# Optimization experiments

Measured on AMD Instinct MI355X. Metric: run time of the kernel, lower is better.

The kernel has to match this reference:

```python
import jax, jax.numpy as jnp
import numpy as np
import math

B, CF, H, W = 2, 64, 256, 256
CH = 32          # 'channel' init arg
KS, DIL, PAD = 3, 2, 2
IMG_H, IMG_W = 512, 512


def _pos_encode(h, w, d_model):
    # Sinusoidal encoding along x and y, interleaved sin/cos -> [2*d_model, h, w]
    div = jnp.exp(jnp.arange(0, d_model, 2, dtype=jnp.float32) * (-math.log(10000.0) / d_model))  # [d/2]
    ax = jnp.arange(w, dtype=jnp.float32)[None, :] * div[:, None]   # [d/2, w]
    ay = jnp.arange(h, dtype=jnp.float32)[None, :] * div[:, None]   # [d/2, h]
    x = jnp.stack([jnp.sin(ax), jnp.cos(ax)], axis=1).reshape(d_model, w)  # even=sin, odd=cos
    y = jnp.stack([jnp.sin(ay), jnp.cos(ay)], axis=1).reshape(d_model, h)
    x = jnp.broadcast_to(x[:, None, :], (d_model, h, w))
    y = jnp.broadcast_to(y[:, :, None], (d_model, h, w))
    return jnp.concatenate([x, y], axis=0)  # [2*d_model, h, w]


def _unfold3x3(x):
    # F.unfold(kernel=3, dilation=2, padding=2, stride=1) -> [B, C, 9, H, W]
    b, c, h, w = x.shape
    xp = jnp.pad(x, ((0, 0), (0, 0), (PAD, PAD), (PAD, PAD)))
    offs = (0, DIL, 2 * DIL)
    patches = [xp[:, :, i:i + h, j:j + w] for i in offs for j in offs]  # row-major kernel order
    return jnp.stack(patches, axis=2)


def setup_inputs() -> dict:
    key = jax.random.key(0)
    k1, k2, k3, k4, k5 = jax.random.split(key, 5)
    return {
        "inp": jax.random.normal(k1, (B, CF, H, W), dtype=jnp.float32),
        "img": jax.random.uniform(k2, (B, 3, IMG_H, IMG_W), dtype=jnp.float32),
        "w_pos": jax.random.normal(k3, (CH, 2 * CH), dtype=jnp.float32) * 0.1,
        "w_img": jax.random.normal(k4, (CH, 3), dtype=jnp.float32) * 0.1,
        "w_comp": jax.random.normal(k5, (CF,), dtype=jnp.float32) * 0.1,
    }


def reference(inp, img, w_pos, w_img, w_comp):
    b, cf, h, w = inp.shape
    # positional embedding -> 1x1 conv (channel matmul)
    pos = _pos_encode(h, w, CH)                                   # [2*CH, H, W]
    pos_embd = jnp.einsum('oc,chw->ohw', w_pos, pos)              # [CH, H, W]
    pos_embd = jnp.broadcast_to(pos_embd[None], (b, CH, h, w))
    # bilinear resize of image to feature resolution, then 1x1 conv
    rimg = jax.image.resize(img, (b, 3, h, w), method='bilinear')
    rimg = jnp.einsum('oc,bchw->bohw', w_img, rimg)               # [B, CH, H, W]
    em = jnp.concatenate([rimg, pos_embd], axis=1)                # [B, 2*CH, H, W]
    # neighborhood similarity score
    un_em = _unfold3x3(em)                                        # [B, 2CH, 9, H, W]
    feature_score = jnp.einsum('bckhw,bchw->bkhw', un_em, em)     # [B, 9, H, W]
    # feature compatibility: 1x1 conv (dot with w_comp) per neighbor, sigmoid
    un_fea = _unfold3x3(inp)                                      # [B, CF, 9, H, W]
    comp_score = jax.nn.sigmoid(jnp.einsum('bckhw,c->bkhw', un_fea, w_comp))
    phi = comp_score * feature_score                              # [B, 9, H, W]
    weighted_fea = jnp.einsum('bckhw,bkhw->bchw', un_fea, phi)    # [B, CF, H, W]
    return weighted_fea
```

## Files before the change

### kernel.cpp

```cpp
#include <hip/hip_runtime.h>
#include <math.h>

namespace {
constexpr int Bn = 2, CF = 64;
constexpr int H = 256, W = 256, HW = H * W;
constexpr int IH = 512, IW = 512;

constexpr int OFF_MT   = 0;
constexpr int OFF_GXX  = OFF_MT + 256 * 256;
constexpr int OFF_GYY  = OFF_GXX + 3 * 256;
constexpr int OFF_G    = OFF_GYY + 3 * 256;
constexpr int OFF_RIMG = OFF_G + 16;
constexpr int OFF_S    = OFF_RIMG + Bn * 3 * HW;
constexpr int OFF_PX   = OFF_RIMG;
constexpr int OFF_PY   = OFF_RIMG + 32 * 256;
}

__global__ __launch_bounds__(256) void pxy_kernel(
    const float* __restrict__ w_pos,
    float* __restrict__ PX, float* __restrict__ PY)
{
  const int t = threadIdx.x;
  const int o = blockIdx.x;
  float s[16], c[16];
#pragma unroll
  for (int i = 0; i < 16; i++) {
    float d = expf((float)(2 * i) * (-0.2878231366242557f));
    float a = (float)t * d;
    s[i] = sinf(a);
    c[i] = cosf(a);
  }
  const float* wr = w_pos + o * 64;
  float ax = 0.f, ay = 0.f;
#pragma unroll
  for (int i = 0; i < 16; i++) {
    ax += wr[2 * i] * s[i] + wr[2 * i + 1] * c[i];
    ay += wr[32 + 2 * i] * s[i] + wr[33 + 2 * i] * c[i];
  }
  PX[o * 256 + t] = ax;
  PY[o * 256 + t] = ay;
}

__global__ __launch_bounds__(256) void gram_kernel(
    const float* __restrict__ PX, const float* __restrict__ PY,
    const float* __restrict__ w_img,
    float* __restrict__ Mt, float* __restrict__ GXX, float* __restrict__ GYY,
    float* __restrict__ G)
{
  const int a = threadIdx.x;
  const int t = blockIdx.x;

  float m = 0.f;
#pragma unroll
  for (int o = 0; o < 32; o++) m += PX[o * 256 + a] * PY[o * 256 + t];
  Mt[t * 256 + a] = m;

  if (t == 0) {
#pragma unroll
    for (int j = 0; j < 3; j++) {
      const int nb = a + 2 * (j - 1);
      float gx = 0.f, gy = 0.f;
      if (nb >= 0 && nb < 256) {
#pragma unroll
        for (int o = 0; o < 32; o++) {
          gx += PX[o * 256 + a] * PX[o * 256 + nb];
          gy += PY[o * 256 + a] * PY[o * 256 + nb];
        }
      }
      GXX[j * 256 + a] = gx;
      GYY[j * 256 + a] = gy;
    }
    if (a < 9) {
      const int i = a / 3, j = a % 3;
      float g = 0.f;
#pragma unroll
      for (int o = 0; o < 32; o++) g += w_img[o * 3 + i] * w_img[o * 3 + j];
      G[a] = g;
    }
  }
}

__device__ __forceinline__ void resize_taps(int p, int n, float w[4], int idx[4])
{
#pragma unroll
  for (int r = 0; r < 4; r++) {
    int q = 2 * p - 1 + r;
    idx[r] = min(max(q, 0), 2 * n - 1);
  }
  if (p == 0)          { w[0] = 0.f;        w[1] = 3.f / 7.f; w[2] = 3.f / 7.f; w[3] = 1.f / 7.f; }
  else if (p == n - 1) { w[0] = 1.f / 7.f;  w[1] = 3.f / 7.f; w[2] = 3.f / 7.f; w[3] = 0.f; }
  else                 { w[0] = 0.125f;     w[1] = 0.375f;    w[2] = 0.375f;    w[3] = 0.125f; }
}

__global__ __launch_bounds__(256) void rimg_kernel(
    const float* __restrict__ img, float* __restrict__ rimg)
{
  const int p = blockIdx.x * 256 + threadIdx.x;
  const int c = blockIdx.y;
  const int b = blockIdx.z;
  const int x = p & (W - 1);
  const int y = p >> 8;

  float wy[4], wx[4];
  int ry[4], rx[4];
  resize_taps(y, H, wy, ry);
  resize_taps(x, W, wx, rx);

  const float* ip = img + ((size_t)(b * 3 + c) * IH) * IW;
  float acc = 0.f;
#pragma unroll
  for (int r = 0; r < 4; r++) {
    const float* rowp = ip + ry[r] * IW;
    float rs = wx[0] * rowp[rx[0]] + wx[1] * rowp[rx[1]] +
               wx[2] * rowp[rx[2]] + wx[3] * rowp[rx[3]];
    acc += wy[r] * rs;
  }
  rimg[((size_t)(b * 3 + c)) * HW + p] = acc;
}

__global__ __launch_bounds__(256) void sigs_kernel(
    const float* __restrict__ inp, const float* __restrict__ w_comp,
    float* __restrict__ sigs)
{
  __shared__ float4 red[256];
  const int lane = threadIdx.x & 63;
  const int cg = threadIdx.x >> 6;
  const int p0 = blockIdx.x * 256 + lane * 4;
  const int b = blockIdx.z;

  const float* ib = inp + (size_t)b * CF * HW + (size_t)cg * 16 * HW + p0;
  float4 acc = {0.f, 0.f, 0.f, 0.f};
#pragma unroll
  for (int c = 0; c < 16; c++) {
    const float4 v = *reinterpret_cast<const float4*>(ib + (size_t)c * HW);
    const float wc = w_comp[cg * 16 + c];
    acc.x += v.x * wc; acc.y += v.y * wc;
    acc.z += v.z * wc; acc.w += v.w * wc;
  }
  red[threadIdx.x] = acc;
  __syncthreads();
  if (threadIdx.x < 64) {
    const float4 a = red[threadIdx.x];
    const float4 b1 = red[threadIdx.x + 64];
    const float4 c1 = red[threadIdx.x + 128];
    const float4 d = red[threadIdx.x + 192];
    float4 s;
    s.x = (a.x + b1.x) + (c1.x + d.x);
    s.y = (a.y + b1.y) + (c1.y + d.y);
    s.z = (a.z + b1.z) + (c1.z + d.z);
    s.w = (a.w + b1.w) + (c1.w + d.w);
    s.x = 1.f / (1.f + expf(-s.x));
    s.y = 1.f / (1.f + expf(-s.y));
    s.z = 1.f / (1.f + expf(-s.z));
    s.w = 1.f / (1.f + expf(-s.w));
    *reinterpret_cast<float4*>(sigs + (size_t)b * HW +
                               blockIdx.x * 256 + threadIdx.x * 4) = s;
  }
}

__global__ __launch_bounds__(256) void phigather_kernel(
    const float* __restrict__ inp, const float* __restrict__ rimg,
    const float* __restrict__ sigs, const float* __restrict__ Mt,
    const float* __restrict__ GXX, const float* __restrict__ GYY,
    const float* __restrict__ G, float* __restrict__ out)
{
  const int cg = blockIdx.x;
  const int p0 = (blockIdx.y * 256 + threadIdx.x) * 4;
  const int b = blockIdx.z;
  const int x0 = p0 & (W - 1);
  const int y  = p0 >> 8;

  const int xl = max(x0 - 2, 0);
  const int xr = min(x0 + 4, W - 2);

  int rowoff[3];
  bool vrow[3];
#pragma unroll
  for (int ky = 0; ky < 3; ky++) {
    const int cy = y + 2 * (ky - 1);
    vrow[ky] = ((unsigned)cy < (unsigned)H);
    rowoff[ky] = min(max(cy, 0), H - 1) * W;
  }

  const float* rb = rimg + (size_t)b * 3 * HW;
  const float* sb = sigs + (size_t)b * HW;

  const float4 r0 = *reinterpret_cast<const float4*>(rb + p0);
  const float4 r1 = *reinterpret_cast<const float4*>(rb + HW + p0);
  const float4 r2 = *reinterpret_cast<const float4*>(rb + 2 * HW + p0);
  float4 t0, t1, t2;
  {
    const float g0 = G[0], g1 = G[1], g2 = G[2];
    const float g3 = G[3], g4 = G[4], g5 = G[5];
    const float g6 = G[6], g7 = G[7], g8 = G[8];
    t0.x = r0.x * g0 + r1.x * g3 + r2.x * g6;
    t0.y = r0.y * g0 + r1.y * g3 + r2.y * g6;
    t0.z = r0.z * g0 + r1.z * g3 + r2.z * g6;
    t0.w = r0.w * g0 + r1.w * g3 + r2.w * g6;
    t1.x = r0.x * g1 + r1.x * g4 + r2.x * g7;
    t1.y = r0.y * g1 + r1.y * g4 + r2.y * g7;
    t1.z = r0.z * g1 + r1.z * g4 + r2.z * g7;
    t1.w = r0.w * g1 + r1.w * g4 + r2.w * g7;
    t2.x = r0.x * g2 + r1.x * g5 + r2.x * g8;
    t2.y = r0.y * g2 + r1.y * g5 + r2.y * g8;
    t2.z = r0.z * g2 + r1.z * g5 + r2.z * g8;
    t2.w = r0.w * g2 + r1.w * g5 + r2.w * g8;
  }

  float mrow[8];
  {
    const float2 L = *reinterpret_cast<const float2*>(Mt + y * W + xl);
    const float4 C = *reinterpret_cast<const float4*>(Mt + y * W + x0);
    const float2 R = *reinterpret_cast<const float2*>(Mt + y * W + xr);
    mrow[0] = L.x; mrow[1] = L.y; mrow[2] = C.x; mrow[3] = C.y;
    mrow[4] = C.z; mrow[5] = C.w; mrow[6] = R.x; mrow[7] = R.y;
  }
  float4 gxxv[3];
#pragma unroll
  for (int kx = 0; kx < 3; kx++)
    gxxv[kx] = *reinterpret_cast<const float4*>(GXX + kx * 256 + x0);

  float4 ph[9];
#pragma unroll
  for (int ky = 0; ky < 3; ky++) {
    const int ro = rowoff[ky];
    float a0[8], a1[8], a2[8], as_[8];
    {
      const float2 L0 = *reinterpret_cast<const float2*>(rb + ro + xl);
      const float4 C0 = *reinterpret_cast<const float4*>(rb + ro + x0);
      const float2 R0 = *reinterpret_cast<const float2*>(rb + ro + xr);
      a0[0]=L0.x; a0[1]=L0.y; a0[2]=C0.x; a0[3]=C0.y;
      a0[4]=C0.z; a0[5]=C0.w; a0[6]=R0.x; a0[7]=R0.y;
      const float2 L1 = *reinterpret_cast<const float2*>(rb + HW + ro + xl);
      const float4 C1 = *reinterpret_cast<const float4*>(rb + HW + ro + x0);
      const float2 R1 = *reinterpret_cast<const float2*>(rb + HW + ro + xr);
      a1[0]=L1.x; a1[1]=L1.y; a1[2]=C1.x; a1[3]=C1.y;
      a1[4]=C1.z; a1[5]=C1.w; a1[6]=R1.x; a1[7]=R1.y;
      const float2 L2 = *reinterpret_cast<const float2*>(rb + 2 * HW + ro + xl);
      const float4 C2 = *reinterpret_cast<const float4*>(rb + 2 * HW + ro + x0);
      const float2 R2 = *reinterpret_cast<const float2*>(rb + 2 * HW + ro + xr);
      a2[0]=L2.x; a2[1]=L2.y; a2[2]=C2.x; a2[3]=C2.y;
      a2[4]=C2.z; a2[5]=C2.w; a2[6]=R2.x; a2[7]=R2.y;
      const float2 Ls = *reinterpret_cast<const float2*>(sb + ro + xl);
      const float4 Cs = *reinterpret_cast<const float4*>(sb + ro + x0);
      const float2 Rs = *reinterpret_cast<const float2*>(sb + ro + xr);
      as_[0]=Ls.x; as_[1]=Ls.y; as_[2]=Cs.x; as_[3]=Cs.y;
      as_[4]=Cs.z; as_[5]=Cs.w; as_[6]=Rs.x; as_[7]=Rs.y;
    }
    const float4 mc = *reinterpret_cast<const float4*>(Mt + ro + x0);
    const float gyy = GYY[ky * 256 + y];

#pragma unroll
    for (int kx = 0; kx < 3; kx++) {
      float4 p;
      {
        const int rel = 0 + 2 * kx;
        const float fs = t0.x * a0[rel] + t1.x * a1[rel] + t2.x * a2[rel]
                       + gxxv[kx].x + gyy + mrow[rel] + mc.x;
        const bool v = vrow[ky] && ((unsigned)(x0 + 0 + 2 * (kx - 1)) < (unsigned)W);
        p.x = v ? as_[rel] * fs : 0.f;
      }
      {
        const int rel = 1 + 2 * kx;
        const float fs = t0.y * a0[rel] + t1.y * a1[rel] + t2.y * a2[rel]
                       + gxxv[kx].y + gyy + mrow[rel] + mc.y;
        const bool v = vrow[ky] && ((unsigned)(x0 + 1 + 2 * (kx - 1)) < (unsigned)W);
        p.y = v ? as_[rel] * fs : 0.f;
      }
      {
        const int rel = 2 + 2 * kx;
        const float fs = t0.z * a0[rel] + t1.z * a1[rel] + t2.z * a2[rel]
                       + gxxv[kx].z + gyy + mrow[rel] + mc.z;
        const bool v = vrow[ky] && ((unsigned)(x0 + 2 + 2 * (kx - 1)) < (unsigned)W);
        p.z = v ? as_[rel] * fs : 0.f;
      }
      {
        const int rel = 3 + 2 * kx;
        const float fs = t0.w * a0[rel] + t1.w * a1[rel] + t2.w * a2[rel]
                       + gxxv[kx].w + gyy + mrow[rel] + mc.w;
        const bool v = vrow[ky] && ((unsigned)(x0 + 3 + 2 * (kx - 1)) < (unsigned)W);
        p.w = v ? as_[rel] * fs : 0.f;
      }
      ph[ky * 3 + kx] = p;
    }
  }

  const float* ib = inp + ((size_t)b * CF + cg * 16) * HW;
  float* ob = out + ((size_t)b * CF + cg * 16) * HW + p0;
#pragma unroll 4
  for (int c = 0; c < 16; c++) {
    const float* ic = ib + (size_t)c * HW;
    float4 acc = {0.f, 0.f, 0.f, 0.f};
#pragma unroll
    for (int ky = 0; ky < 3; ky++) {
      const int ro = rowoff[ky];
      const float2 L = *reinterpret_cast<const float2*>(ic + ro + xl);
      const float4 C = *reinterpret_cast<const float4*>(ic + ro + x0);
      const float2 R = *reinterpret_cast<const float2*>(ic + ro + xr);
      const float a[8] = {L.x, L.y, C.x, C.y, C.z, C.w, R.x, R.y};
#pragma unroll
      for (int kx = 0; kx < 3; kx++) {
        const float4 w = ph[ky * 3 + kx];
        acc.x += w.x * a[0 + 2 * kx];
        acc.y += w.y * a[1 + 2 * kx];
        acc.z += w.z * a[2 + 2 * kx];
        acc.w += w.w * a[3 + 2 * kx];
      }
    }
    *reinterpret_cast<float4*>(ob + (size_t)c * HW) = acc;
  }
}

extern "C" void kernel_launch(void* const* d_in, const int* in_sizes, int n_in,
                              void* d_out, int out_size, void* d_ws, size_t ws_size,
                              hipStream_t stream)
{
  const float* inp    = (const float*)d_in[0];
  const float* img    = (const float*)d_in[1];
  const float* w_pos  = (const float*)d_in[2];
  const float* w_img  = (const float*)d_in[3];
  const float* w_comp = (const float*)d_in[4];
  float* out = (float*)d_out;
  float* ws  = (float*)d_ws;

  float* Mt   = ws + OFF_MT;
  float* GXX  = ws + OFF_GXX;
  float* GYY  = ws + OFF_GYY;
  float* G    = ws + OFF_G;
  float* rimg = ws + OFF_RIMG;
  float* sigs = ws + OFF_S;
  float* PX   = ws + OFF_PX;
  float* PY   = ws + OFF_PY;

  hipLaunchKernelGGL(pxy_kernel, dim3(32), dim3(256), 0, stream, w_pos, PX, PY);
  hipLaunchKernelGGL(gram_kernel, dim3(256), dim3(256), 0, stream,
                     PX, PY, w_img, Mt, GXX, GYY, G);

  hipLaunchKernelGGL(rimg_kernel, dim3(HW / 256, 3, Bn), dim3(256), 0, stream,
                     img, rimg);
  hipLaunchKernelGGL(sigs_kernel, dim3(HW / 256, 1, Bn), dim3(256), 0, stream,
                     inp, w_comp, sigs);

  hipLaunchKernelGGL(phigather_kernel, dim3(CF / 16, HW / 1024, Bn), dim3(256), 0, stream,
                     inp, rimg, sigs, Mt, GXX, GYY, G, out);
}
```

Baseline: 134.6 us.

## Merge resize and sigmoid kernels, halve channels per phigather block

The separate rimg and sigs kernels become one prep kernel with a flat grid: the first range of blocks does the bilinear resize and the rest compute the sigmoid compatibility score. The sigs part now has each thread handle one pixel with scalar loads and four independent accumulators, which gives four times as many blocks. The phigather kernel now handles 8 channels per block instead of 16 and launches 8 channel groups, doubling the block count. Recomputing the phi weights per block becomes twice as redundant in exchange for more parallelism and one fewer launch.

```diff
diff --git a/kernel.cpp b/kernel.cpp
--- a/kernel.cpp
+++ b/kernel.cpp
@@ -14,6 +14,9 @@
 constexpr int OFF_S    = OFF_RIMG + Bn * 3 * HW;
 constexpr int OFF_PX   = OFF_RIMG;
 constexpr int OFF_PY   = OFF_RIMG + 32 * 256;
+
+constexpr int RIMG_BLOCKS = Bn * 3 * (HW / 256);
+constexpr int SIGS_BLOCKS = Bn * (HW / 64);
 }
 
 __global__ __launch_bounds__(256) void pxy_kernel(
@@ -92,69 +95,61 @@
   else                 { w[0] = 0.125f;     w[1] = 0.375f;    w[2] = 0.375f;    w[3] = 0.125f; }
 }
 
-__global__ __launch_bounds__(256) void rimg_kernel(
-    const float* __restrict__ img, float* __restrict__ rimg)
-{
-  const int p = blockIdx.x * 256 + threadIdx.x;
-  const int c = blockIdx.y;
-  const int b = blockIdx.z;
-  const int x = p & (W - 1);
-  const int y = p >> 8;
-
-  float wy[4], wx[4];
-  int ry[4], rx[4];
-  resize_taps(y, H, wy, ry);
-  resize_taps(x, W, wx, rx);
-
-  const float* ip = img + ((size_t)(b * 3 + c) * IH) * IW;
-  float acc = 0.f;
-#pragma unroll
-  for (int r = 0; r < 4; r++) {
-    const float* rowp = ip + ry[r] * IW;
-    float rs = wx[0] * rowp[rx[0]] + wx[1] * rowp[rx[1]] +
-               wx[2] * rowp[rx[2]] + wx[3] * rowp[rx[3]];
-    acc += wy[r] * rs;
-  }
-  rimg[((size_t)(b * 3 + c)) * HW + p] = acc;
-}
-
-__global__ __launch_bounds__(256) void sigs_kernel(
-    const float* __restrict__ inp, const float* __restrict__ w_comp,
-    float* __restrict__ sigs)
-{
-  __shared__ float4 red[256];
-  const int lane = threadIdx.x & 63;
-  const int cg = threadIdx.x >> 6;
-  const int p0 = blockIdx.x * 256 + lane * 4;
-  const int b = blockIdx.z;
-
-  const float* ib = inp + (size_t)b * CF * HW + (size_t)cg * 16 * HW + p0;
-  float4 acc = {0.f, 0.f, 0.f, 0.f};
-#pragma unroll
-  for (int c = 0; c < 16; c++) {
-    const float4 v = *reinterpret_cast<const float4*>(ib + (size_t)c * HW);
-    const float wc = w_comp[cg * 16 + c];
-    acc.x += v.x * wc; acc.y += v.y * wc;
-    acc.z += v.z * wc; acc.w += v.w * wc;
-  }
-  red[threadIdx.x] = acc;
-  __syncthreads();
-  if (threadIdx.x < 64) {
-    const float4 a = red[threadIdx.x];
-    const float4 b1 = red[threadIdx.x + 64];
-    const float4 c1 = red[threadIdx.x + 128];
-    const float4 d = red[threadIdx.x + 192];
-    float4 s;
-    s.x = (a.x + b1.x) + (c1.x + d.x);
-    s.y = (a.y + b1.y) + (c1.y + d.y);
-    s.z = (a.z + b1.z) + (c1.z + d.z);
-    s.w = (a.w + b1.w) + (c1.w + d.w);
-    s.x = 1.f / (1.f + expf(-s.x));
-    s.y = 1.f / (1.f + expf(-s.y));
-    s.z = 1.f / (1.f + expf(-s.z));
-    s.w = 1.f / (1.f + expf(-s.w));
-    *reinterpret_cast<float4*>(sigs + (size_t)b * HW +
-                               blockIdx.x * 256 + threadIdx.x * 4) = s;
+__global__ __launch_bounds__(256) void prep_kernel(
+    const float* __restrict__ img, const float* __restrict__ inp,
+    const float* __restrict__ w_comp,
+    float* __restrict__ rimg, float* __restrict__ sigs)
+{
+  __shared__ float red[256];
+  const int gid = blockIdx.x;
+
+  if (gid < RIMG_BLOCKS) {
+    const int b = gid / 768;
+    const int rem = gid % 768;
+    const int c = rem / 256;
+    const int p = (rem % 256) * 256 + threadIdx.x;
+    const int x = p & (W - 1);
+    const int y = p >> 8;
+
+    float wy[4], wx[4];
+    int ry[4], rx[4];
+    resize_taps(y, H, wy, ry);
+    resize_taps(x, W, wx, rx);
+
+    const float* ip = img + ((size_t)(b * 3 + c) * IH) * IW;
+    float acc = 0.f;
+#pragma unroll
+    for (int r = 0; r < 4; r++) {
+      const float* rowp = ip + ry[r] * IW;
+      float rs = wx[0] * rowp[rx[0]] + wx[1] * rowp[rx[1]] +
+                 wx[2] * rowp[rx[2]] + wx[3] * rowp[rx[3]];
+      acc += wy[r] * rs;
+    }
+    rimg[((size_t)(b * 3 + c)) * HW + p] = acc;
+  } else {
+    const int j = gid - RIMG_BLOCKS;
+    const int b = j / (HW / 64);
+    const int pblk = j % (HW / 64);
+    const int lane = threadIdx.x & 63;
+    const int cg = threadIdx.x >> 6;
+    const int p = pblk * 64 + lane;
+
+    const float* ib = inp + (size_t)b * CF * HW + (size_t)cg * 16 * HW + p;
+    float a0 = 0.f, a1 = 0.f, a2 = 0.f, a3 = 0.f;
+#pragma unroll
+    for (int c = 0; c < 16; c += 4) {
+      a0 += ib[(size_t)(c + 0) * HW] * w_comp[cg * 16 + c + 0];
+      a1 += ib[(size_t)(c + 1) * HW] * w_comp[cg * 16 + c + 1];
+      a2 += ib[(size_t)(c + 2) * HW] * w_comp[cg * 16 + c + 2];
+      a3 += ib[(size_t)(c + 3) * HW] * w_comp[cg * 16 + c + 3];
+    }
+    red[threadIdx.x] = (a0 + a1) + (a2 + a3);
+    __syncthreads();
+    if (threadIdx.x < 64) {
+      const float s = red[threadIdx.x] + red[threadIdx.x + 64] +
+                      red[threadIdx.x + 128] + red[threadIdx.x + 192];
+      sigs[(size_t)b * HW + pblk * 64 + threadIdx.x] = 1.f / (1.f + expf(-s));
+    }
   }
 }
 
@@ -285,10 +280,10 @@
     }
   }
 
-  const float* ib = inp + ((size_t)b * CF + cg * 16) * HW;
-  float* ob = out + ((size_t)b * CF + cg * 16) * HW + p0;
+  const float* ib = inp + ((size_t)b * CF + cg * 8) * HW;
+  float* ob = out + ((size_t)b * CF + cg * 8) * HW + p0;
 #pragma unroll 4
-  for (int c = 0; c < 16; c++) {
+  for (int c = 0; c < 8; c++) {
     const float* ic = ib + (size_t)c * HW;
     float4 acc = {0.f, 0.f, 0.f, 0.f};
 #pragma unroll
@@ -336,11 +331,9 @@
   hipLaunchKernelGGL(gram_kernel, dim3(256), dim3(256), 0, stream,
                      PX, PY, w_img, Mt, GXX, GYY, G);
 
-  hipLaunchKernelGGL(rimg_kernel, dim3(HW / 256, 3, Bn), dim3(256), 0, stream,
-                     img, rimg);
-  hipLaunchKernelGGL(sigs_kernel, dim3(HW / 256, 1, Bn), dim3(256), 0, stream,
-                     inp, w_comp, sigs);
-
-  hipLaunchKernelGGL(phigather_kernel, dim3(CF / 16, HW / 1024, Bn), dim3(256), 0, stream,
+  hipLaunchKernelGGL(prep_kernel, dim3(RIMG_BLOCKS + SIGS_BLOCKS), dim3(256), 0, stream,
+                     img, inp, w_comp, rimg, sigs);
+
+  hipLaunchKernelGGL(phigather_kernel, dim3(8, HW / 1024, Bn), dim3(256), 0, stream,
                      inp, rimg, sigs, Mt, GXX, GYY, G, out);
 }
```

New measurement: 121.7 us. 9.6% less time.

## Merge gram, resize and sigmoid prep kernels into one launch; halve gather channel groups

Applied to the files above, without the earlier changes.

Combines the gram, image-resize and compatibility-sigmoid kernels into a single block-indexed prep kernel and moves PX/PY to their own workspace region so they no longer alias rimg. The aim is to cut launch count and the serialization between small kernels. It also splits the final gather into 8 channel groups of 8 channels instead of 4 groups of 16, which doubles parallelism but also doubles the redundant per-pixel phi computation.

```diff
diff --git a/kernel.cpp b/kernel.cpp
--- a/kernel.cpp
+++ b/kernel.cpp
@@ -12,8 +12,13 @@
 constexpr int OFF_G    = OFF_GYY + 3 * 256;
 constexpr int OFF_RIMG = OFF_G + 16;
 constexpr int OFF_S    = OFF_RIMG + Bn * 3 * HW;
-constexpr int OFF_PX   = OFF_RIMG;
-constexpr int OFF_PY   = OFF_RIMG + 32 * 256;
+constexpr int OFF_PX   = OFF_S + Bn * HW;
+constexpr int OFF_PY   = OFF_PX + 32 * 256;
+
+constexpr int GRAM_BLOCKS = 256;
+constexpr int RIMG_BLOCKS = Bn * 3 * (HW / 256);
+constexpr int SIGS_BLOCKS = Bn * (HW / 256);
+constexpr int PREP_BLOCKS = GRAM_BLOCKS + RIMG_BLOCKS + SIGS_BLOCKS;
 }
 
 __global__ __launch_bounds__(256) void pxy_kernel(
@@ -41,45 +46,6 @@
   PY[o * 256 + t] = ay;
 }
 
-__global__ __launch_bounds__(256) void gram_kernel(
-    const float* __restrict__ PX, const float* __restrict__ PY,
-    const float* __restrict__ w_img,
-    float* __restrict__ Mt, float* __restrict__ GXX, float* __restrict__ GYY,
-    float* __restrict__ G)
-{
-  const int a = threadIdx.x;
-  const int t = blockIdx.x;
-
-  float m = 0.f;
-#pragma unroll
-  for (int o = 0; o < 32; o++) m += PX[o * 256 + a] * PY[o * 256 + t];
-  Mt[t * 256 + a] = m;
-
-  if (t == 0) {
-#pragma unroll
-    for (int j = 0; j < 3; j++) {
-      const int nb = a + 2 * (j - 1);
-      float gx = 0.f, gy = 0.f;
-      if (nb >= 0 && nb < 256) {
-#pragma unroll
-        for (int o = 0; o < 32; o++) {
-          gx += PX[o * 256 + a] * PX[o * 256 + nb];
-          gy += PY[o * 256 + a] * PY[o * 256 + nb];
-        }
-      }
-      GXX[j * 256 + a] = gx;
-      GYY[j * 256 + a] = gy;
-    }
-    if (a < 9) {
-      const int i = a / 3, j = a % 3;
-      float g = 0.f;
-#pragma unroll
-      for (int o = 0; o < 32; o++) g += w_img[o * 3 + i] * w_img[o * 3 + j];
-      G[a] = g;
-    }
-  }
-}
-
 __device__ __forceinline__ void resize_taps(int p, int n, float w[4], int idx[4])
 {
 #pragma unroll
@@ -92,69 +58,109 @@
   else                 { w[0] = 0.125f;     w[1] = 0.375f;    w[2] = 0.375f;    w[3] = 0.125f; }
 }
 
-__global__ __launch_bounds__(256) void rimg_kernel(
-    const float* __restrict__ img, float* __restrict__ rimg)
-{
-  const int p = blockIdx.x * 256 + threadIdx.x;
-  const int c = blockIdx.y;
-  const int b = blockIdx.z;
-  const int x = p & (W - 1);
-  const int y = p >> 8;
-
-  float wy[4], wx[4];
-  int ry[4], rx[4];
-  resize_taps(y, H, wy, ry);
-  resize_taps(x, W, wx, rx);
-
-  const float* ip = img + ((size_t)(b * 3 + c) * IH) * IW;
-  float acc = 0.f;
-#pragma unroll
-  for (int r = 0; r < 4; r++) {
-    const float* rowp = ip + ry[r] * IW;
-    float rs = wx[0] * rowp[rx[0]] + wx[1] * rowp[rx[1]] +
-               wx[2] * rowp[rx[2]] + wx[3] * rowp[rx[3]];
-    acc += wy[r] * rs;
-  }
-  rimg[((size_t)(b * 3 + c)) * HW + p] = acc;
-}
-
-__global__ __launch_bounds__(256) void sigs_kernel(
-    const float* __restrict__ inp, const float* __restrict__ w_comp,
-    float* __restrict__ sigs)
-{
-  __shared__ float4 red[256];
-  const int lane = threadIdx.x & 63;
-  const int cg = threadIdx.x >> 6;
-  const int p0 = blockIdx.x * 256 + lane * 4;
-  const int b = blockIdx.z;
-
-  const float* ib = inp + (size_t)b * CF * HW + (size_t)cg * 16 * HW + p0;
-  float4 acc = {0.f, 0.f, 0.f, 0.f};
-#pragma unroll
-  for (int c = 0; c < 16; c++) {
-    const float4 v = *reinterpret_cast<const float4*>(ib + (size_t)c * HW);
-    const float wc = w_comp[cg * 16 + c];
-    acc.x += v.x * wc; acc.y += v.y * wc;
-    acc.z += v.z * wc; acc.w += v.w * wc;
-  }
-  red[threadIdx.x] = acc;
-  __syncthreads();
-  if (threadIdx.x < 64) {
-    const float4 a = red[threadIdx.x];
-    const float4 b1 = red[threadIdx.x + 64];
-    const float4 c1 = red[threadIdx.x + 128];
-    const float4 d = red[threadIdx.x + 192];
-    float4 s;
-    s.x = (a.x + b1.x) + (c1.x + d.x);
-    s.y = (a.y + b1.y) + (c1.y + d.y);
-    s.z = (a.z + b1.z) + (c1.z + d.z);
-    s.w = (a.w + b1.w) + (c1.w + d.w);
-    s.x = 1.f / (1.f + expf(-s.x));
-    s.y = 1.f / (1.f + expf(-s.y));
-    s.z = 1.f / (1.f + expf(-s.z));
-    s.w = 1.f / (1.f + expf(-s.w));
-    *reinterpret_cast<float4*>(sigs + (size_t)b * HW +
-                               blockIdx.x * 256 + threadIdx.x * 4) = s;
+__global__ __launch_bounds__(256) void prep_kernel(
+    const float* __restrict__ img, const float* __restrict__ inp,
+    const float* __restrict__ w_comp, const float* __restrict__ w_img,
+    const float* __restrict__ PX, const float* __restrict__ PY,
+    float* __restrict__ rimg, float* __restrict__ sigs,
+    float* __restrict__ Mt, float* __restrict__ GXX, float* __restrict__ GYY,
+    float* __restrict__ G)
+{
+  __shared__ float4 red4[256];
+  const int gid = blockIdx.x;
+
+  if (gid < GRAM_BLOCKS) {
+    const int a = threadIdx.x;
+    const int t = gid;
+
+    float m = 0.f;
+#pragma unroll
+    for (int o = 0; o < 32; o++) m += PX[o * 256 + a] * PY[o * 256 + t];
+    Mt[t * 256 + a] = m;
+
+    if (t == 0) {
+#pragma unroll
+      for (int j = 0; j < 3; j++) {
+        const int nb = a + 2 * (j - 1);
+        float gx = 0.f, gy = 0.f;
+        if (nb >= 0 && nb < 256) {
+#pragma unroll
+          for (int o = 0; o < 32; o++) {
+            gx += PX[o * 256 + a] * PX[o * 256 + nb];
+            gy += PY[o * 256 + a] * PY[o * 256 + nb];
+          }
+        }
+        GXX[j * 256 + a] = gx;
+        GYY[j * 256 + a] = gy;
+      }
+      if (a < 9) {
+        const int i = a / 3, j = a % 3;
+        float g = 0.f;
+#pragma unroll
+        for (int o = 0; o < 32; o++) g += w_img[o * 3 + i] * w_img[o * 3 + j];
+        G[a] = g;
+      }
+    }
+  } else if (gid < GRAM_BLOCKS + RIMG_BLOCKS) {
+    const int rid = gid - GRAM_BLOCKS;
+    const int b = rid / 768;
+    const int rem = rid % 768;
+    const int c = rem / 256;
+    const int p = (rem % 256) * 256 + threadIdx.x;
+    const int x = p & (W - 1);
+    const int y = p >> 8;
+
+    float wy[4], wx[4];
+    int ry[4], rx[4];
+    resize_taps(y, H, wy, ry);
+    resize_taps(x, W, wx, rx);
+
+    const float* ip = img + ((size_t)(b * 3 + c) * IH) * IW;
+    float acc = 0.f;
+#pragma unroll
+    for (int r = 0; r < 4; r++) {
+      const float* rowp = ip + ry[r] * IW;
+      float rs = wx[0] * rowp[rx[0]] + wx[1] * rowp[rx[1]] +
+                 wx[2] * rowp[rx[2]] + wx[3] * rowp[rx[3]];
+      acc += wy[r] * rs;
+    }
+    rimg[((size_t)(b * 3 + c)) * HW + p] = acc;
+  } else {
+    const int sid = gid - (GRAM_BLOCKS + RIMG_BLOCKS);
+    const int b = sid / (HW / 256);
+    const int pblk = sid % (HW / 256);
+    const int lane = threadIdx.x & 63;
+    const int cg = threadIdx.x >> 6;
+    const int p0 = pblk * 256 + lane * 4;
+
+    const float* ib = inp + (size_t)b * CF * HW + (size_t)cg * 16 * HW + p0;
+    float4 acc = {0.f, 0.f, 0.f, 0.f};
+#pragma unroll
+    for (int c = 0; c < 16; c++) {
+      const float4 v = *reinterpret_cast<const float4*>(ib + (size_t)c * HW);
+      const float wc = w_comp[cg * 16 + c];
+      acc.x += v.x * wc; acc.y += v.y * wc;
+      acc.z += v.z * wc; acc.w += v.w * wc;
+    }
+    red4[threadIdx.x] = acc;
+    __syncthreads();
+    if (threadIdx.x < 64) {
+      const float4 a = red4[threadIdx.x];
+      const float4 b1 = red4[threadIdx.x + 64];
+      const float4 c1 = red4[threadIdx.x + 128];
+      const float4 d = red4[threadIdx.x + 192];
+      float4 s;
+      s.x = (a.x + b1.x) + (c1.x + d.x);
+      s.y = (a.y + b1.y) + (c1.y + d.y);
+      s.z = (a.z + b1.z) + (c1.z + d.z);
+      s.w = (a.w + b1.w) + (c1.w + d.w);
+      s.x = 1.f / (1.f + expf(-s.x));
+      s.y = 1.f / (1.f + expf(-s.y));
+      s.z = 1.f / (1.f + expf(-s.z));
+      s.w = 1.f / (1.f + expf(-s.w));
+      *reinterpret_cast<float4*>(sigs + (size_t)b * HW +
+                                 pblk * 256 + threadIdx.x * 4) = s;
+    }
   }
 }
 
@@ -285,10 +291,10 @@
     }
   }
 
-  const float* ib = inp + ((size_t)b * CF + cg * 16) * HW;
-  float* ob = out + ((size_t)b * CF + cg * 16) * HW + p0;
+  const float* ib = inp + ((size_t)b * CF + cg * 8) * HW;
+  float* ob = out + ((size_t)b * CF + cg * 8) * HW + p0;
 #pragma unroll 4
-  for (int c = 0; c < 16; c++) {
+  for (int c = 0; c < 8; c++) {
     const float* ic = ib + (size_t)c * HW;
     float4 acc = {0.f, 0.f, 0.f, 0.f};
 #pragma unroll
@@ -333,14 +339,11 @@
   float* PY   = ws + OFF_PY;
 
   hipLaunchKernelGGL(pxy_kernel, dim3(32), dim3(256), 0, stream, w_pos, PX, PY);
-  hipLaunchKernelGGL(gram_kernel, dim3(256), dim3(256), 0, stream,
-                     PX, PY, w_img, Mt, GXX, GYY, G);
-
-  hipLaunchKernelGGL(rimg_kernel, dim3(HW / 256, 3, Bn), dim3(256), 0, stream,
-                     img, rimg);
-  hipLaunchKernelGGL(sigs_kernel, dim3(HW / 256, 1, Bn), dim3(256), 0, stream,
-                     inp, w_comp, sigs);
-
-  hipLaunchKernelGGL(phigather_kernel, dim3(CF / 16, HW / 1024, Bn), dim3(256), 0, stream,
+
+  hipLaunchKernelGGL(prep_kernel, dim3(PREP_BLOCKS), dim3(256), 0, stream,
+                     img, inp, w_comp, w_img, PX, PY,
+                     rimg, sigs, Mt, GXX, GYY, G);
+
+  hipLaunchKernelGGL(phigather_kernel, dim3(8, HW / 1024, Bn), dim3(256), 0, stream,
                      inp, rimg, sigs, Mt, GXX, GYY, G, out);
 }
```

New measurement: 118.6 us. 1.13x faster.
